# Performance work log

Hardware: AMD Instinct MI355X
Metric: run time of the kernel (lower is better)

The kernel has to match this reference:

```python
import jax, jax.numpy as jnp
import numpy as np

# dims (match init_kwargs)
S = 2048      # sequence_length
H = 2048      # hidden_size
NH = 32       # num_attention_heads
KVH = 8       # num_key_value_heads
HD = 64       # head_dim
WIN = 128     # sliding_window
QM = NH // KVH
SM_SCALE = 1.0 / float(np.sqrt(HD))


def _rope_rotate(x, cos, sin):
    # x: [S, n, HD]; cos/sin: [S, HD//2]
    x1, x2 = jnp.split(x, 2, axis=-1)
    c = cos[:, None, :].astype(x.dtype)
    s = sin[:, None, :].astype(x.dtype)
    return jnp.concatenate([x1 * c - x2 * s, x2 * c + x1 * s], axis=-1)


def setup_inputs() -> dict:
    key = jax.random.key(0)
    ks = jax.random.split(key, 6)
    x = jax.random.normal(ks[0], (S, H), jnp.float32)
    qkv_dim = HD * (NH + 2 * KVH)
    qkv_kernel = jax.random.normal(ks[1], (H, qkv_dim), jnp.float32) * 0.02
    qkv_bias = jnp.zeros((qkv_dim,), jnp.float32)
    out_kernel = jax.random.normal(ks[2], (NH * HD, H), jnp.float32) * 0.02
    out_bias = jnp.zeros((H,), jnp.float32)
    sinks = jax.random.normal(ks[3], (NH,), jnp.float32) * 0.02
    # RoPE tables: [S, HD//2]
    pos = np.arange(S, dtype=np.float32)
    inv_freq = 1.0 / (10000.0 ** (np.arange(HD // 2, dtype=np.float32) / (HD // 2)))
    ang = pos[:, None] * inv_freq[None, :]
    cos_table = jnp.asarray(np.cos(ang), jnp.float32)
    sin_table = jnp.asarray(np.sin(ang), jnp.float32)
    # causal + sliding-window additive mask [S, S]
    qi = np.arange(S, dtype=np.int32)[:, None]
    ki = np.arange(S, dtype=np.int32)[None, :]
    m = np.where(ki > qi, -np.inf, 0.0).astype(np.float32)
    m = np.where(ki < qi - WIN, -np.inf, m).astype(np.float32)
    mask = jnp.asarray(m)
    return {"x": x, "qkv_kernel": qkv_kernel, "qkv_bias": qkv_bias,
            "out_kernel": out_kernel, "out_bias": out_bias, "sinks": sinks,
            "cos_table": cos_table, "sin_table": sin_table, "mask": mask}


def reference(x, qkv_kernel, qkv_bias, out_kernel, out_bias, sinks, cos_table, sin_table, mask):
    xf = x.astype(jnp.float32)
    qkv = jnp.dot(xf, qkv_kernel, precision=jax.lax.Precision.HIGHEST) + qkv_bias  # [S, qkv_dim]
    q_end = NH * HD
    k_end = q_end + KVH * HD
    q = qkv[:, :q_end].reshape(S, NH, HD)          # NH = KVH*QM
    k = qkv[:, q_end:k_end].reshape(S, KVH, HD)
    v = qkv[:, k_end:].reshape(S, KVH, HD)
    q = _rope_rotate(q, cos_table, sin_table).reshape(S, KVH, QM, HD)
    k = _rope_rotate(k, cos_table, sin_table)
    # logits: [KVH, QM, S_q, S_k]; K broadcast across q_mult (GQA)
    logits = jnp.einsum('qhmd,khd->hmqk', q, k) * jnp.float32(SM_SCALE)
    logits = logits + mask[None, None, :, :]
    sink = jnp.broadcast_to(sinks.reshape(KVH, QM, 1, 1).astype(jnp.float32), (KVH, QM, S, 1))
    extended = jnp.concatenate([logits, sink], axis=-1)
    weights = jax.nn.softmax(extended, axis=-1)[..., :-1]
    attn = jnp.einsum('hmqk,khd->qhmd', weights, v).reshape(S, NH * HD)
    out = jnp.dot(attn, out_kernel, precision=jax.lax.Precision.HIGHEST) + out_bias
    return out.astype(x.dtype)
```

## Files before the change

### kernel.cpp

```cpp
#include <hip/hip_runtime.h>
#include <hip/hip_bf16.h>
#include <cstdint>

typedef __hip_bfloat16 bf16;
typedef __attribute__((ext_vector_type(8))) __bf16 bf16x8;
typedef __attribute__((ext_vector_type(4))) float f32x4;

static __device__ __forceinline__ void gload_lds16(const void* g, void* l) {
  __builtin_amdgcn_global_load_lds(
      (const __attribute__((address_space(1))) uint32_t*)g,
      (__attribute__((address_space(3))) uint32_t*)l, 16, 0, 0);
}

__global__ __launch_bounds__(256)
void prep_kernel(const float* __restrict__ x, const float* __restrict__ w1,
                 const float* __restrict__ w2, bf16* __restrict__ xb,
                 bf16* __restrict__ w1t, bf16* __restrict__ w2t) {
  __shared__ float tile[32][33];
  const int lin = blockIdx.x;
  const int t = threadIdx.x;
  if (lin < 4096) {
    const int i = lin * 256 + t;
    const float4 v = reinterpret_cast<const float4*>(x)[i];
    ushort4 o;
    o.x = __builtin_bit_cast(unsigned short, __float2bfloat16(v.x));
    o.y = __builtin_bit_cast(unsigned short, __float2bfloat16(v.y));
    o.z = __builtin_bit_cast(unsigned short, __float2bfloat16(v.z));
    o.w = __builtin_bit_cast(unsigned short, __float2bfloat16(v.w));
    reinterpret_cast<ushort4*>(xb)[i] = o;
    return;
  }
  const float* in;
  bf16* out;
  int R, C, bx, by;
  if (lin < 10240) {
    const int tl = lin - 4096;
    in = w1; out = w1t; R = 2048; C = 3072; bx = tl % 96; by = tl / 96;
  } else {
    const int tl = lin - 10240;
    in = w2; out = w2t; R = 2048; C = 2048; bx = tl & 63; by = tl >> 6;
  }
  const int c0 = bx * 32, r0 = by * 32;
  const int tx = t & 31, ty = t >> 5;
#pragma unroll
  for (int i = 0; i < 4; ++i)
    tile[ty + i * 8][tx] = in[(size_t)(r0 + ty + i * 8) * C + c0 + tx];
  __syncthreads();
#pragma unroll
  for (int i = 0; i < 4; ++i)
    out[(size_t)(c0 + ty + i * 8) * R + r0 + tx] = __float2bfloat16(tile[tx][ty + i * 8]);
}

template <int NH, int SSHIFT>
__global__ void rope_kernel(bf16* __restrict__ buf, const float* __restrict__ cosT,
                            const float* __restrict__ sinT) {
  const int idx = blockIdx.x * 256 + threadIdx.x;
  const int c = idx & 3;
  const int h = (idx >> 2) & (NH - 1);
  const int s = idx >> SSHIFT;
  bf16* p = buf + (size_t)s * (NH * 64) + h * 64 + c * 8;
  bf16x8 v1 = *reinterpret_cast<bf16x8*>(p);
  bf16x8 v2 = *reinterpret_cast<bf16x8*>(p + 32);
  const float4 c0 = *reinterpret_cast<const float4*>(&cosT[s * 32 + c * 8]);
  const float4 c1 = *reinterpret_cast<const float4*>(&cosT[s * 32 + c * 8 + 4]);
  const float4 s0 = *reinterpret_cast<const float4*>(&sinT[s * 32 + c * 8]);
  const float4 s1 = *reinterpret_cast<const float4*>(&sinT[s * 32 + c * 8 + 4]);
  const float cs[8] = {c0.x, c0.y, c0.z, c0.w, c1.x, c1.y, c1.z, c1.w};
  const float sn[8] = {s0.x, s0.y, s0.z, s0.w, s1.x, s1.y, s1.z, s1.w};
  bf16x8 o1, o2;
#pragma unroll
  for (int e = 0; e < 8; ++e) {
    const float x1 = (float)v1[e], x2 = (float)v2[e];
    o1[e] = (__bf16)(x1 * cs[e] - x2 * sn[e]);
    o2[e] = (__bf16)(x2 * cs[e] + x1 * sn[e]);
  }
  *reinterpret_cast<bf16x8*>(p) = o1;
  *reinterpret_cast<bf16x8*>(p + 32) = o2;
}

__global__ __launch_bounds__(512, 1)
void gemm1_kernel(const bf16* __restrict__ A, const bf16* __restrict__ Bt,
                  const float* __restrict__ bias,
                  bf16* __restrict__ qb, bf16* __restrict__ kb, bf16* __restrict__ vt) {
  extern __shared__ __align__(16) char smem[];
  constexpr int K = 2048, NK = 32;
  const int lin = blockIdx.x;
  const int wgid = (lin & 7) * 32 + (lin >> 3);
  const int bx = wgid >> 4, by = wgid & 15;
  const int brow = by * 128, bcol = bx * 192;
  const int t = threadIdx.x, lane = t & 63, w = t >> 6;
  const int wr = w >> 2, wc = w & 3;
  const int rr = lane & 15, rg = lane >> 4;

  char* Ab = smem;
  char* Bb = smem + 49152;

  auto stageA = [&](int kt) {
#pragma unroll
    for (int p = 0; p < 2; ++p) {
      const int idx = p * 512 + t;
      const int row = idx >> 3;
      const int cg = (idx & 7) ^ (row & 7);
      gload_lds16(A + (size_t)(brow + row) * K + kt * 64 + cg * 8,
                  Ab + (size_t)(kt % 3) * 16384 + (p * 512 + (t & ~63)) * 16);
    }
  };
  auto stageB = [&](int kt) {
#pragma unroll
    for (int p = 0; p < 3; ++p) {
      const int idx = p * 512 + t;
      const int row = idx >> 3;
      const int cg = (idx & 7) ^ (row & 7);
      gload_lds16(Bt + (size_t)(bcol + row) * K + kt * 64 + cg * 8,
                  Bb + (size_t)(kt % 3) * 24576 + (p * 512 + (t & ~63)) * 16);
    }
  };

  f32x4 acc[4][3];
#pragma unroll
  for (int i = 0; i < 4; ++i)
#pragma unroll
    for (int j = 0; j < 3; ++j) acc[i][j] = f32x4{0.f, 0.f, 0.f, 0.f};

  stageA(0); stageB(0); stageA(1); stageB(1);
  asm volatile("s_waitcnt vmcnt(5)" ::: "memory");
  __builtin_amdgcn_s_barrier();

  for (int kt = 0; kt < NK; ++kt) {
    const char* Ar = Ab + (size_t)(kt % 3) * 16384;
    const char* Br = Bb + (size_t)(kt % 3) * 24576;
#pragma unroll
    for (int ks = 0; ks < 2; ++ks) {
      bf16x8 af[4], bfr[3];
      const int c = ks * 4 + rg;
#pragma unroll
      for (int i = 0; i < 4; ++i) {
        const int row = wr * 64 + i * 16 + rr;
        af[i] = *reinterpret_cast<const bf16x8*>(Ar + row * 128 + ((c ^ (row & 7)) * 16));
      }
#pragma unroll
      for (int j = 0; j < 3; ++j) {
        const int row = wc * 48 + j * 16 + rr;
        bfr[j] = *reinterpret_cast<const bf16x8*>(Br + row * 128 + ((c ^ (row & 7)) * 16));
      }
      if (kt + 2 < NK) {
        if (ks == 0) stageA(kt + 2);
        else         stageB(kt + 2);
      }
      asm volatile("s_waitcnt lgkmcnt(0)" ::: "memory");
      __builtin_amdgcn_sched_barrier(0);
      __builtin_amdgcn_s_setprio(1);
#pragma unroll
      for (int i = 0; i < 4; ++i)
#pragma unroll
        for (int j = 0; j < 3; ++j)
          acc[i][j] = __builtin_amdgcn_mfma_f32_16x16x32_bf16(af[i], bfr[j], acc[i][j], 0, 0, 0);
      __builtin_amdgcn_s_setprio(0);
    }
    if (kt + 2 < NK)      asm volatile("s_waitcnt vmcnt(5)" ::: "memory");
    else if (kt + 1 < NK) asm volatile("s_waitcnt vmcnt(0)" ::: "memory");
    if (kt + 1 < NK) __builtin_amdgcn_s_barrier();
  }

#pragma unroll
  for (int j = 0; j < 3; ++j) {
    const int gcf = bcol + wc * 48 + j * 16;
    const int gc = gcf + rr;
    const float bv = bias[gc];
    if (gcf < 2048) {
#pragma unroll
      for (int i = 0; i < 4; ++i) {
        const int s0 = brow + wr * 64 + i * 16 + rg * 4;
#pragma unroll
        for (int r = 0; r < 4; ++r)
          qb[(size_t)(s0 + r) * 2048 + gc] = __float2bfloat16(acc[i][j][r] + bv);
      }
    } else if (gcf < 2560) {
      const int kc = gc - 2048;
#pragma unroll
      for (int i = 0; i < 4; ++i) {
        const int s0 = brow + wr * 64 + i * 16 + rg * 4;
#pragma unroll
        for (int r = 0; r < 4; ++r)
          kb[(size_t)(s0 + r) * 512 + kc] = __float2bfloat16(acc[i][j][r] + bv);
      }
    } else {
      const int vcol = gc - 2560;
#pragma unroll
      for (int i = 0; i < 4; ++i) {
        ushort4 o;
        o.x = __builtin_bit_cast(unsigned short, __float2bfloat16(acc[i][j][0] + bv));
        o.y = __builtin_bit_cast(unsigned short, __float2bfloat16(acc[i][j][1] + bv));
        o.z = __builtin_bit_cast(unsigned short, __float2bfloat16(acc[i][j][2] + bv));
        o.w = __builtin_bit_cast(unsigned short, __float2bfloat16(acc[i][j][3] + bv));
        *reinterpret_cast<ushort4*>(
            &vt[(size_t)vcol * 2048 + brow + wr * 64 + i * 16 + rg * 4]) = o;
      }
    }
  }
}

__global__ __launch_bounds__(512, 1)
void gemm2_kernel(const bf16* __restrict__ A, const bf16* __restrict__ Bt,
                  const float* __restrict__ bias, float* __restrict__ C) {
  extern __shared__ __align__(16) char smem[];
  constexpr int K = 2048, NK = 32;
  const int lin = blockIdx.x;
  const int wgid = (lin & 7) * 32 + (lin >> 3);
  const int bx = wgid >> 4, by = wgid & 15;
  const int brow = by * 128, bcol = bx * 128;
  const int t = threadIdx.x, lane = t & 63, w = t >> 6;
  const int wr = w & 3, wc = w >> 2;
  const int rr = lane & 15, rg = lane >> 4;

  char* Ab = smem;
  char* Bb = smem + 49152;

  auto stage = [&](int kt) {
#pragma unroll
    for (int p = 0; p < 2; ++p) {
      const int idx = p * 512 + t;
      const int row = idx >> 3;
      const int cg = (idx & 7) ^ (row & 7);
      gload_lds16(A + (size_t)(brow + row) * K + kt * 64 + cg * 8,
                  Ab + (size_t)(kt % 3) * 16384 + (p * 512 + (t & ~63)) * 16);
      gload_lds16(Bt + (size_t)(bcol + row) * K + kt * 64 + cg * 8,
                  Bb + (size_t)(kt % 3) * 16384 + (p * 512 + (t & ~63)) * 16);
    }
  };

  f32x4 acc[2][4];
#pragma unroll
  for (int i = 0; i < 2; ++i)
#pragma unroll
    for (int j = 0; j < 4; ++j) acc[i][j] = f32x4{0.f, 0.f, 0.f, 0.f};

  stage(0); stage(1);
  asm volatile("s_waitcnt vmcnt(4)" ::: "memory");
  __builtin_amdgcn_s_barrier();

  for (int kt = 0; kt < NK; ++kt) {
    const char* Ar = Ab + (size_t)(kt % 3) * 16384;
    const char* Br = Bb + (size_t)(kt % 3) * 16384;
#pragma unroll
    for (int ks = 0; ks < 2; ++ks) {
      bf16x8 af[2], bfr[4];
      const int c = ks * 4 + rg;
#pragma unroll
      for (int i = 0; i < 2; ++i) {
        const int row = wr * 32 + i * 16 + rr;
        af[i] = *reinterpret_cast<const bf16x8*>(Ar + row * 128 + ((c ^ (row & 7)) * 16));
      }
#pragma unroll
      for (int j = 0; j < 4; ++j) {
        const int row = wc * 64 + j * 16 + rr;
        bfr[j] = *reinterpret_cast<const bf16x8*>(Br + row * 128 + ((c ^ (row & 7)) * 16));
      }
      if (kt + 2 < NK && ks == 0) stage(kt + 2);
      asm volatile("s_waitcnt lgkmcnt(0)" ::: "memory");
      __builtin_amdgcn_sched_barrier(0);
      __builtin_amdgcn_s_setprio(1);
#pragma unroll
      for (int i = 0; i < 2; ++i)
#pragma unroll
        for (int j = 0; j < 4; ++j)
          acc[i][j] = __builtin_amdgcn_mfma_f32_16x16x32_bf16(af[i], bfr[j], acc[i][j], 0, 0, 0);
      __builtin_amdgcn_s_setprio(0);
    }
    if (kt + 2 < NK)      asm volatile("s_waitcnt vmcnt(4)" ::: "memory");
    else if (kt + 1 < NK) asm volatile("s_waitcnt vmcnt(0)" ::: "memory");
    if (kt + 1 < NK) __builtin_amdgcn_s_barrier();
  }

#pragma unroll
  for (int i = 0; i < 2; ++i)
#pragma unroll
    for (int j = 0; j < 4; ++j) {
      const int gc = bcol + wc * 64 + j * 16 + rr;
      const float bv = bias[gc];
      const int r0 = brow + wr * 32 + i * 16 + rg * 4;
#pragma unroll
      for (int r = 0; r < 4; ++r)
        C[(size_t)(r0 + r) * 2048 + gc] = acc[i][j][r] + bv;
    }
}

__global__ __launch_bounds__(256, 2)
void attn_kernel(const bf16* __restrict__ Q, const bf16* __restrict__ Kb,
                 const bf16* __restrict__ Vt, const float* __restrict__ sinks,
                 const float* __restrict__ cosT, const float* __restrict__ sinT,
                 bf16* __restrict__ aout) {
  extern __shared__ __align__(16) char smem[];
  const int hk = blockIdx.x;
  const int q0 = blockIdx.y * 32;
  const int k0 = q0 - 128;
  const int t = threadIdx.x, w = t >> 6, lane = t & 63;
  const int cl = lane & 15, rg = lane >> 4;
  const int head = hk * 4 + w;

  char* Ks = smem;
  char* Vs = smem;
  char* Ps = smem + 20480 + w * 12288;

#pragma unroll
  for (int p = 0; p < 5; ++p) {
    const int idx = p * 256 + t;
    const int row = idx >> 3, c = idx & 7;
    int key = k0 + row;
    if (key < 0) key = 0;
    gload_lds16(Kb + (size_t)key * 512 + hk * 64 + ((c ^ (row & 7)) << 3),
                Ks + (size_t)(p * 256 + (t & ~63)) * 16);
  }

  bf16x8 aq[2][2];
#pragma unroll
  for (int qf = 0; qf < 2; ++qf) {
    const int qrow = q0 + qf * 16 + cl;
    const bf16* qp = Q + (size_t)qrow * 2048 + head * 64 + rg * 8;
    const bf16x8 q1 = *reinterpret_cast<const bf16x8*>(qp);
    const bf16x8 q2 = *reinterpret_cast<const bf16x8*>(qp + 32);
    const float4 c0 = *reinterpret_cast<const float4*>(&cosT[qrow * 32 + rg * 8]);
    const float4 c1 = *reinterpret_cast<const float4*>(&cosT[qrow * 32 + rg * 8 + 4]);
    const float4 s0 = *reinterpret_cast<const float4*>(&sinT[qrow * 32 + rg * 8]);
    const float4 s1 = *reinterpret_cast<const float4*>(&sinT[qrow * 32 + rg * 8 + 4]);
    const float cs[8] = {c0.x, c0.y, c0.z, c0.w, c1.x, c1.y, c1.z, c1.w};
    const float sn[8] = {s0.x, s0.y, s0.z, s0.w, s1.x, s1.y, s1.z, s1.w};
#pragma unroll
    for (int e = 0; e < 8; ++e) {
      const float x1 = (float)q1[e], x2 = (float)q2[e];
      aq[qf][0][e] = (__bf16)(x1 * cs[e] - x2 * sn[e]);
      aq[qf][1][e] = (__bf16)(x2 * cs[e] + x1 * sn[e]);
    }
  }
  __syncthreads();

  f32x4 acc[2][10];
#pragma unroll
  for (int qf = 0; qf < 2; ++qf)
#pragma unroll
    for (int nf = 0; nf < 10; ++nf) acc[qf][nf] = f32x4{0.f, 0.f, 0.f, 0.f};

#pragma unroll
  for (int nf = 0; nf < 10; ++nf) {
    const int row = nf * 16 + cl;
    bf16x8 bk[2];
#pragma unroll
    for (int ks = 0; ks < 2; ++ks) {
      const int chunk = ks * 4 + rg;
      bk[ks] = *reinterpret_cast<const bf16x8*>(
          Ks + row * 128 + ((chunk ^ (row & 7)) << 4));
    }
#pragma unroll
    for (int qf = 0; qf < 2; ++qf)
#pragma unroll
      for (int ks = 0; ks < 2; ++ks)
        acc[qf][nf] = __builtin_amdgcn_mfma_f32_16x16x32_bf16(aq[qf][ks], bk[ks], acc[qf][nf], 0, 0, 0);
  }

  __syncthreads();

  {
    const bf16* vbase = Vt + (size_t)hk * 64 * 2048;
#pragma unroll
    for (int p = 0; p < 5; ++p) {
      const int idx = p * 256 + t;
      const int row = idx / 20;
      const int slot = idx - row * 20;
      int src = slot - (row & 7);
      if (src < 0) src += 20;
      int key = k0 + src * 8;
      if (key < 0) key = 0;
      gload_lds16(vbase + (size_t)row * 2048 + key,
                  Vs + (size_t)(p * 256 + (t & ~63)) * 16);
    }
  }

  const float sinkv = sinks[head];
  const float scale = 0.125f;
  const int cfloor = 128 - q0;
#pragma unroll
  for (int qf = 0; qf < 2; ++qf)
#pragma unroll
    for (int r = 0; r < 4; ++r) {
      const int rowb = qf * 16 + rg * 4 + r;
      int cmin = rowb;
      if (cfloor > cmin) cmin = cfloor;
      const int cmax = rowb + 128;
      float m = sinkv;
      float pv[10];
#pragma unroll
      for (int nf = 0; nf < 10; ++nf) {
        const int cc = nf * 16 + cl;
        float lv = (cc >= cmin && cc <= cmax) ? acc[qf][nf][r] * scale : -INFINITY;
        pv[nf] = lv;
        m = fmaxf(m, lv);
      }
#pragma unroll
      for (int off = 1; off < 16; off <<= 1)
        m = fmaxf(m, __shfl_xor(m, off, 64));
      float sum = 0.f;
#pragma unroll
      for (int nf = 0; nf < 10; ++nf) {
        const float p = __expf(pv[nf] - m);
        pv[nf] = p;
        sum += p;
      }
#pragma unroll
      for (int off = 1; off < 16; off <<= 1)
        sum += __shfl_xor(sum, off, 64);
      sum += __expf(sinkv - m);
      const float inv = 1.f / sum;
#pragma unroll
      for (int nf = 0; nf < 10; ++nf) {
        const int col = nf * 16 + cl;
        const int chunk = col >> 3;
        *reinterpret_cast<bf16*>(Ps + rowb * 384 + ((chunk ^ (rowb & 7)) << 4) + (cl & 7) * 2) =
            __float2bfloat16(pv[nf] * inv);
      }
    }

  asm volatile("s_waitcnt vmcnt(0) lgkmcnt(0)" ::: "memory");
  __builtin_amdgcn_sched_barrier(0);
  __syncthreads();

  f32x4 oacc[2][4];
#pragma unroll
  for (int qf = 0; qf < 2; ++qf)
#pragma unroll
    for (int j = 0; j < 4; ++j) oacc[qf][j] = f32x4{0.f, 0.f, 0.f, 0.f};

#pragma unroll
  for (int ks = 0; ks < 5; ++ks) {
    bf16x8 pa[2];
#pragma unroll
    for (int qf = 0; qf < 2; ++qf) {
      const int row = qf * 16 + cl;
      const int chunk = ks * 4 + rg;
      pa[qf] = *reinterpret_cast<const bf16x8*>(
          Ps + row * 384 + ((chunk ^ (row & 7)) << 4));
    }
#pragma unroll
    for (int j = 0; j < 4; ++j) {
      const int d = j * 16 + cl;
      int slot = ks * 4 + rg + (d & 7);
      if (slot >= 20) slot -= 20;
      const bf16x8 bv = *reinterpret_cast<const bf16x8*>(Vs + d * 320 + slot * 16);
#pragma unroll
      for (int qf = 0; qf < 2; ++qf)
        oacc[qf][j] = __builtin_amdgcn_mfma_f32_16x16x32_bf16(pa[qf], bv, oacc[qf][j], 0, 0, 0);
    }
  }

#pragma unroll
  for (int qf = 0; qf < 2; ++qf)
#pragma unroll
    for (int j = 0; j < 4; ++j)
#pragma unroll
      for (int r = 0; r < 4; ++r) {
        const int row = qf * 16 + rg * 4 + r;
        const int colb = (j * 16 + cl) * 2;
        *reinterpret_cast<bf16*>(Ps + row * 384 + (colb ^ ((row & 7) << 4))) =
            __float2bfloat16(oacc[qf][j][r]);
      }
  __syncthreads();

#pragma unroll
  for (int p = 0; p < 4; ++p) {
    const int idx = p * 256 + t;
    const int row = idx >> 5;
    const int j16 = idx & 31;
    const int w2 = j16 >> 3, c8 = j16 & 7;
    const uint4 v = *reinterpret_cast<const uint4*>(
        smem + 20480 + w2 * 12288 + row * 384 + ((c8 * 16) ^ ((row & 7) << 4)));
    *reinterpret_cast<uint4*>(aout + (size_t)(q0 + row) * 2048 + hk * 256 + j16 * 8) = v;
  }
}

extern "C" void kernel_launch(void* const* d_in, const int* in_sizes, int n_in,
                              void* d_out, int out_size, void* d_ws, size_t ws_size,
                              hipStream_t stream) {
  const float* x     = (const float*)d_in[0];
  const float* w1    = (const float*)d_in[1];
  const float* b1    = (const float*)d_in[2];
  const float* w2    = (const float*)d_in[3];
  const float* b2    = (const float*)d_in[4];
  const float* sinks = (const float*)d_in[5];
  const float* cosT  = (const float*)d_in[6];
  const float* sinT  = (const float*)d_in[7];
  float* out = (float*)d_out;

  char* ws = (char*)d_ws;
  bf16* xb   = (bf16*)(ws);
  bf16* w1t  = (bf16*)(ws + 8388608);
  bf16* w2t  = (bf16*)(ws + 20971520);
  bf16* qbuf = (bf16*)(ws + 29360128);
  bf16* kbuf = (bf16*)(ws + 37748736);
  bf16* vt   = (bf16*)(ws + 39845888);
  bf16* attn = (bf16*)(ws + 41943040);
  (void)in_sizes; (void)n_in; (void)out_size; (void)ws_size;

  prep_kernel<<<14336, 256, 0, stream>>>(x, w1, w2, xb, w1t, w2t);
  gemm1_kernel<<<256, 512, 122880, stream>>>(xb, w1t, b1, qbuf, kbuf, vt);
  rope_kernel<8, 5><<<256, 256, 0, stream>>>(kbuf, cosT, sinT);
  attn_kernel<<<dim3(8, 64), 256, 69632, stream>>>(qbuf, kbuf, vt, sinks, cosT, sinT, attn);
  gemm2_kernel<<<256, 512, 98304, stream>>>(attn, w2t, b2, out);
}
```

Before: 85.79 us.

## Fuse K RoPE into attention kernel and shrink QKV GEMM tiles to 64 rows

Removes the separate K RoPE kernel launch and instead rotates the K tile inside the attention kernel after it is loaded into shared memory. This recomputes RoPE for overlapping key windows across query blocks but saves one launch and a global read/write pass. The QKV GEMM tile height drops from 128 to 64 rows, doubling the grid to 512 blocks. The pipeline changes from triple to double buffering with 64 KB LDS, aiming for better CU occupancy and wave balance at the cost of less reuse and a shallower prefetch.

```diff
diff --git a/kernel.cpp b/kernel.cpp
--- a/kernel.cpp
+++ b/kernel.cpp
@@ -51,59 +51,28 @@
     out[(size_t)(c0 + ty + i * 8) * R + r0 + tx] = __float2bfloat16(tile[tx][ty + i * 8]);
 }
 
-template <int NH, int SSHIFT>
-__global__ void rope_kernel(bf16* __restrict__ buf, const float* __restrict__ cosT,
-                            const float* __restrict__ sinT) {
-  const int idx = blockIdx.x * 256 + threadIdx.x;
-  const int c = idx & 3;
-  const int h = (idx >> 2) & (NH - 1);
-  const int s = idx >> SSHIFT;
-  bf16* p = buf + (size_t)s * (NH * 64) + h * 64 + c * 8;
-  bf16x8 v1 = *reinterpret_cast<bf16x8*>(p);
-  bf16x8 v2 = *reinterpret_cast<bf16x8*>(p + 32);
-  const float4 c0 = *reinterpret_cast<const float4*>(&cosT[s * 32 + c * 8]);
-  const float4 c1 = *reinterpret_cast<const float4*>(&cosT[s * 32 + c * 8 + 4]);
-  const float4 s0 = *reinterpret_cast<const float4*>(&sinT[s * 32 + c * 8]);
-  const float4 s1 = *reinterpret_cast<const float4*>(&sinT[s * 32 + c * 8 + 4]);
-  const float cs[8] = {c0.x, c0.y, c0.z, c0.w, c1.x, c1.y, c1.z, c1.w};
-  const float sn[8] = {s0.x, s0.y, s0.z, s0.w, s1.x, s1.y, s1.z, s1.w};
-  bf16x8 o1, o2;
-#pragma unroll
-  for (int e = 0; e < 8; ++e) {
-    const float x1 = (float)v1[e], x2 = (float)v2[e];
-    o1[e] = (__bf16)(x1 * cs[e] - x2 * sn[e]);
-    o2[e] = (__bf16)(x2 * cs[e] + x1 * sn[e]);
-  }
-  *reinterpret_cast<bf16x8*>(p) = o1;
-  *reinterpret_cast<bf16x8*>(p + 32) = o2;
-}
-
-__global__ __launch_bounds__(512, 1)
+__global__ __launch_bounds__(512, 4)
 void gemm1_kernel(const bf16* __restrict__ A, const bf16* __restrict__ Bt,
                   const float* __restrict__ bias,
                   bf16* __restrict__ qb, bf16* __restrict__ kb, bf16* __restrict__ vt) {
   extern __shared__ __align__(16) char smem[];
   constexpr int K = 2048, NK = 32;
   const int lin = blockIdx.x;
-  const int wgid = (lin & 7) * 32 + (lin >> 3);
-  const int bx = wgid >> 4, by = wgid & 15;
-  const int brow = by * 128, bcol = bx * 192;
+  const int wgid = (lin & 7) * 64 + (lin >> 3);
+  const int bx = wgid >> 5, by = wgid & 31;
+  const int brow = by * 64, bcol = bx * 192;
   const int t = threadIdx.x, lane = t & 63, w = t >> 6;
   const int wr = w >> 2, wc = w & 3;
   const int rr = lane & 15, rg = lane >> 4;
 
   char* Ab = smem;
-  char* Bb = smem + 49152;
+  char* Bb = smem + 16384;
 
   auto stageA = [&](int kt) {
-#pragma unroll
-    for (int p = 0; p < 2; ++p) {
-      const int idx = p * 512 + t;
-      const int row = idx >> 3;
-      const int cg = (idx & 7) ^ (row & 7);
-      gload_lds16(A + (size_t)(brow + row) * K + kt * 64 + cg * 8,
-                  Ab + (size_t)(kt % 3) * 16384 + (p * 512 + (t & ~63)) * 16);
-    }
+    const int row = t >> 3;
+    const int cg = (t & 7) ^ (row & 7);
+    gload_lds16(A + (size_t)(brow + row) * K + kt * 64 + cg * 8,
+                Ab + (size_t)(kt & 1) * 8192 + (t & ~63) * 16);
   };
   auto stageB = [&](int kt) {
 #pragma unroll
@@ -112,30 +81,30 @@
       const int row = idx >> 3;
       const int cg = (idx & 7) ^ (row & 7);
       gload_lds16(Bt + (size_t)(bcol + row) * K + kt * 64 + cg * 8,
-                  Bb + (size_t)(kt % 3) * 24576 + (p * 512 + (t & ~63)) * 16);
+                  Bb + (size_t)(kt & 1) * 24576 + (p * 512 + (t & ~63)) * 16);
     }
   };
 
-  f32x4 acc[4][3];
-#pragma unroll
-  for (int i = 0; i < 4; ++i)
+  f32x4 acc[2][3];
+#pragma unroll
+  for (int i = 0; i < 2; ++i)
 #pragma unroll
     for (int j = 0; j < 3; ++j) acc[i][j] = f32x4{0.f, 0.f, 0.f, 0.f};
 
-  stageA(0); stageB(0); stageA(1); stageB(1);
-  asm volatile("s_waitcnt vmcnt(5)" ::: "memory");
+  stageA(0); stageB(0);
+  asm volatile("s_waitcnt vmcnt(0)" ::: "memory");
   __builtin_amdgcn_s_barrier();
 
   for (int kt = 0; kt < NK; ++kt) {
-    const char* Ar = Ab + (size_t)(kt % 3) * 16384;
-    const char* Br = Bb + (size_t)(kt % 3) * 24576;
+    const char* Ar = Ab + (size_t)(kt & 1) * 8192;
+    const char* Br = Bb + (size_t)(kt & 1) * 24576;
 #pragma unroll
     for (int ks = 0; ks < 2; ++ks) {
-      bf16x8 af[4], bfr[3];
+      bf16x8 af[2], bfr[3];
       const int c = ks * 4 + rg;
 #pragma unroll
-      for (int i = 0; i < 4; ++i) {
-        const int row = wr * 64 + i * 16 + rr;
+      for (int i = 0; i < 2; ++i) {
+        const int row = wr * 32 + i * 16 + rr;
         af[i] = *reinterpret_cast<const bf16x8*>(Ar + row * 128 + ((c ^ (row & 7)) * 16));
       }
 #pragma unroll
@@ -143,23 +112,21 @@
         const int row = wc * 48 + j * 16 + rr;
         bfr[j] = *reinterpret_cast<const bf16x8*>(Br + row * 128 + ((c ^ (row & 7)) * 16));
       }
-      if (kt + 2 < NK) {
-        if (ks == 0) stageA(kt + 2);
-        else         stageB(kt + 2);
-      }
+      if (ks == 0 && kt + 1 < NK) { stageA(kt + 1); stageB(kt + 1); }
       asm volatile("s_waitcnt lgkmcnt(0)" ::: "memory");
       __builtin_amdgcn_sched_barrier(0);
       __builtin_amdgcn_s_setprio(1);
 #pragma unroll
-      for (int i = 0; i < 4; ++i)
+      for (int i = 0; i < 2; ++i)
 #pragma unroll
         for (int j = 0; j < 3; ++j)
           acc[i][j] = __builtin_amdgcn_mfma_f32_16x16x32_bf16(af[i], bfr[j], acc[i][j], 0, 0, 0);
       __builtin_amdgcn_s_setprio(0);
     }
-    if (kt + 2 < NK)      asm volatile("s_waitcnt vmcnt(5)" ::: "memory");
-    else if (kt + 1 < NK) asm volatile("s_waitcnt vmcnt(0)" ::: "memory");
-    if (kt + 1 < NK) __builtin_amdgcn_s_barrier();
+    if (kt + 1 < NK) {
+      asm volatile("s_waitcnt vmcnt(0)" ::: "memory");
+      __builtin_amdgcn_s_barrier();
+    }
   }
 
 #pragma unroll
@@ -169,8 +136,8 @@
     const float bv = bias[gc];
     if (gcf < 2048) {
 #pragma unroll
-      for (int i = 0; i < 4; ++i) {
-        const int s0 = brow + wr * 64 + i * 16 + rg * 4;
+      for (int i = 0; i < 2; ++i) {
+        const int s0 = brow + wr * 32 + i * 16 + rg * 4;
 #pragma unroll
         for (int r = 0; r < 4; ++r)
           qb[(size_t)(s0 + r) * 2048 + gc] = __float2bfloat16(acc[i][j][r] + bv);
@@ -178,8 +145,8 @@
     } else if (gcf < 2560) {
       const int kc = gc - 2048;
 #pragma unroll
-      for (int i = 0; i < 4; ++i) {
-        const int s0 = brow + wr * 64 + i * 16 + rg * 4;
+      for (int i = 0; i < 2; ++i) {
+        const int s0 = brow + wr * 32 + i * 16 + rg * 4;
 #pragma unroll
         for (int r = 0; r < 4; ++r)
           kb[(size_t)(s0 + r) * 512 + kc] = __float2bfloat16(acc[i][j][r] + bv);
@@ -187,14 +154,14 @@
     } else {
       const int vcol = gc - 2560;
 #pragma unroll
-      for (int i = 0; i < 4; ++i) {
+      for (int i = 0; i < 2; ++i) {
         ushort4 o;
         o.x = __builtin_bit_cast(unsigned short, __float2bfloat16(acc[i][j][0] + bv));
         o.y = __builtin_bit_cast(unsigned short, __float2bfloat16(acc[i][j][1] + bv));
         o.z = __builtin_bit_cast(unsigned short, __float2bfloat16(acc[i][j][2] + bv));
         o.w = __builtin_bit_cast(unsigned short, __float2bfloat16(acc[i][j][3] + bv));
         *reinterpret_cast<ushort4*>(
-            &vt[(size_t)vcol * 2048 + brow + wr * 64 + i * 16 + rg * 4]) = o;
+            &vt[(size_t)vcol * 2048 + brow + wr * 32 + i * 16 + rg * 4]) = o;
       }
     }
   }
@@ -334,6 +301,37 @@
   }
   __syncthreads();
 
+#pragma unroll
+  for (int p = 0; p < 3; ++p) {
+    const int task = p * 256 + t;
+    if (task < 640) {
+      const int row = task >> 2, c = task & 3;
+      int key = k0 + row;
+      if (key < 0) key = 0;
+      char* base = Ks + row * 128;
+      const int slotA = (c ^ (row & 7)) << 4;
+      const int slotB = ((c + 4) ^ (row & 7)) << 4;
+      bf16x8 v1 = *reinterpret_cast<bf16x8*>(base + slotA);
+      bf16x8 v2 = *reinterpret_cast<bf16x8*>(base + slotB);
+      const float4 ca0 = *reinterpret_cast<const float4*>(&cosT[key * 32 + c * 8]);
+      const float4 ca1 = *reinterpret_cast<const float4*>(&cosT[key * 32 + c * 8 + 4]);
+      const float4 sa0 = *reinterpret_cast<const float4*>(&sinT[key * 32 + c * 8]);
+      const float4 sa1 = *reinterpret_cast<const float4*>(&sinT[key * 32 + c * 8 + 4]);
+      const float cs[8] = {ca0.x, ca0.y, ca0.z, ca0.w, ca1.x, ca1.y, ca1.z, ca1.w};
+      const float sn[8] = {sa0.x, sa0.y, sa0.z, sa0.w, sa1.x, sa1.y, sa1.z, sa1.w};
+      bf16x8 o1, o2;
+#pragma unroll
+      for (int e = 0; e < 8; ++e) {
+        const float x1 = (float)v1[e], x2 = (float)v2[e];
+        o1[e] = (__bf16)(x1 * cs[e] - x2 * sn[e]);
+        o2[e] = (__bf16)(x2 * cs[e] + x1 * sn[e]);
+      }
+      *reinterpret_cast<bf16x8*>(base + slotA) = o1;
+      *reinterpret_cast<bf16x8*>(base + slotB) = o2;
+    }
+  }
+  __syncthreads();
+
   f32x4 acc[2][10];
 #pragma unroll
   for (int qf = 0; qf < 2; ++qf)
@@ -500,8 +498,7 @@
   (void)in_sizes; (void)n_in; (void)out_size; (void)ws_size;
 
   prep_kernel<<<14336, 256, 0, stream>>>(x, w1, w2, xb, w1t, w2t);
-  gemm1_kernel<<<256, 512, 122880, stream>>>(xb, w1t, b1, qbuf, kbuf, vt);
-  rope_kernel<8, 5><<<256, 256, 0, stream>>>(kbuf, cosT, sinT);
+  gemm1_kernel<<<512, 512, 65536, stream>>>(xb, w1t, b1, qbuf, kbuf, vt);
   attn_kernel<<<dim3(8, 64), 256, 69632, stream>>>(qbuf, kbuf, vt, sinks, cosT, sinT, attn);
   gemm2_kernel<<<256, 512, 98304, stream>>>(attn, w2t, b2, out);
 }
```

Result: no change. 86.73 us (+1.1%).
